# Kernel tuning notes

Hardware: AMD Instinct MI355X
Metric: run time of the kernel (lower is better)

## Reference

```python
import jax, jax.numpy as jnp
import numpy as np

N_NODES = 50000
N_EDGES = 800000
MAX_ITER = 20  # torchdeq default f_max_iter=40; fixed iteration count for a tractable jit-able baseline
K = 3          # TAGConv default number of hops
INS, EMB, HID, OUT = 4, 64, 128, 1


def setup_inputs():
    key = jax.random.key(0)
    ks = jax.random.split(key, 12)
    def lin(k, fan_in, fan_out):
        return jax.random.normal(k, (fan_in, fan_out), jnp.float32) / np.sqrt(fan_in)
    def tag_w(k, fan_in, fan_out):
        # stacked weights for the K+1 TAGConv linear maps: [K+1, in, out]
        return jax.random.normal(k, (K + 1, fan_in, fan_out), jnp.float32) / np.sqrt(fan_in * (K + 1))
    return {
        "x": jax.random.normal(ks[0], (N_NODES, INS), jnp.float32),
        "pos": jax.random.normal(ks[1], (N_NODES, 3), jnp.float32),
        "edge_attr": jax.random.uniform(ks[2], (N_EDGES,), jnp.float32),
        "up_w1": lin(ks[3], INS, EMB), "up_b1": jnp.zeros((EMB,), jnp.float32),
        "up_w2": lin(ks[4], EMB, EMB), "up_b2": jnp.zeros((EMB,), jnp.float32),
        "c1_w": tag_w(ks[5], EMB + 3, HID), "c1_b": jnp.zeros((HID,), jnp.float32),
        "c2_w": tag_w(ks[6], HID, HID), "c2_b": jnp.zeros((HID,), jnp.float32),
        "c3_w": tag_w(ks[7], HID, EMB), "c3_b": jnp.zeros((EMB,), jnp.float32),
        "down_w1": lin(ks[8], EMB, OUT), "down_b1": jnp.zeros((OUT,), jnp.float32),
        "down_w2": lin(ks[9], OUT, OUT), "down_b2": jnp.zeros((OUT,), jnp.float32),
        "edge_index": jax.random.randint(ks[10], (2, N_EDGES), 0, N_NODES, jnp.int32),
    }


def _gcn_norm(row, col, edge_attr, n):
    # PyG gcn_norm with edge weights, no self loops (TAGConv default)
    deg = jax.ops.segment_sum(edge_attr, col, num_segments=n)
    safe = jnp.where(deg > 0, deg, 1.0)
    dinv = jnp.where(deg > 0, jax.lax.rsqrt(safe), 0.0)
    return dinv[row] * edge_attr * dinv[col]


def _mlp(x, w1, b1, w2, b2):
    # torch F.gelu default = exact erf gelu
    return jax.nn.gelu(x @ w1 + b1, approximate=False) @ w2 + b2


def reference(x, pos, edge_attr, up_w1, up_b1, up_w2, up_b2, c1_w, c1_b, c2_w, c2_b, c3_w, c3_b, down_w1, down_b1, down_w2, down_b2, edge_index):
    n = x.shape[0]
    row, col = edge_index[0], edge_index[1]
    norm = _gcn_norm(row, col, edge_attr, n)

    def tag(h, W, b):
        # TAGConv: sum_k lin_k( A_hat^k x ) + bias
        out = h @ W[0]
        for k in range(1, W.shape[0]):
            h = jax.ops.segment_sum(h[row] * norm[:, None], col, num_segments=n)  # [E,C] gather-scatter
            out = out + h @ W[k]
        return out + b

    def gnn(z):
        h = jnp.concatenate([z, pos], axis=1)
        h = jax.nn.relu(tag(h, c1_w, c1_b))
        h = jax.nn.relu(tag(h, c2_w, c2_b))  # F.dropout is identity in eval mode
        h = tag(h, c3_w, c3_b)
        return jax.nn.log_softmax(h, axis=1)

    z0 = _mlp(x, up_w1, up_b1, up_w2, up_b2)
    z = jax.lax.fori_loop(0, MAX_ITER, lambda i, zz: gnn(zz), z0)  # fixed-point solver
    z_star = gnn(z)  # phantom-gradient step (torchdeq grad=1)
    out = _mlp(z_star, down_w1, down_b1, down_w2, down_b2)
    return out, z_star
```

## Files before the change

### kernel.cpp

```cpp
#include <hip/hip_runtime.h>
#include <hip/hip_bf16.h>

#define N_NODES 50000
#define N_EDGES 800000
#define MAX_ITER 20

typedef __attribute__((ext_vector_type(8))) short bf16x8;
typedef __attribute__((ext_vector_type(4))) float f32x4;

__device__ __forceinline__ float gelu_f(float x){
  return 0.5f*x*(1.0f+erff(x*0.70710678118654752f));
}
__device__ __forceinline__ ushort f2b(float f){
  uint x = __float_as_uint(f);
  uint r = (x + 0x7fffu + ((x>>16)&1u)) >> 16;
  return (ushort)r;
}

__global__ void deg_cnt_kernel(const int* __restrict__ col, const float* __restrict__ attr,
                               float* __restrict__ deg, int* __restrict__ cnt){
  int e = blockIdx.x*256 + threadIdx.x;
  if (e < N_EDGES){
    int c = col[e];
    atomicAdd(&deg[c], attr[e]);
    atomicAdd(&cnt[c], 1);
  }
}

__global__ void norm_kernel(const int* __restrict__ row, const int* __restrict__ col,
                            const float* __restrict__ attr, const float* __restrict__ deg,
                            float* __restrict__ nrm){
  int e = blockIdx.x*256 + threadIdx.x;
  if (e < N_EDGES){
    float dr = deg[row[e]], dc = deg[col[e]];
    float ir = dr > 0.f ? rsqrtf(dr) : 0.f;
    float ic = dc > 0.f ? rsqrtf(dc) : 0.f;
    nrm[e] = ir * attr[e] * ic;
  }
}

__global__ void scan_kernel(const int* __restrict__ cnt, int* __restrict__ starts,
                            int* __restrict__ cursor){
  __shared__ int buf[1024];
  __shared__ int carry;
  int tid = threadIdx.x;
  if (tid==0) carry = 0;
  __syncthreads();
  for (int base=0; base<N_NODES; base+=1024){
    int i = base+tid;
    int v = (i<N_NODES)? cnt[i] : 0;
    int cv = carry;
    buf[tid]=v;
    __syncthreads();
    for (int off=1; off<1024; off<<=1){
      int t = (tid>=off)? buf[tid-off] : 0;
      __syncthreads();
      buf[tid]+=t;
      __syncthreads();
    }
    int excl = buf[tid]-v+cv;
    if (i<N_NODES){ starts[i]=excl; cursor[i]=excl; }
    __syncthreads();
    if (tid==0) carry = cv + buf[1023];
    __syncthreads();
  }
  if (tid==0) starts[N_NODES] = carry;
}

__global__ void fill_kernel(const int* __restrict__ row, const int* __restrict__ col,
                            const float* __restrict__ nrm, int* __restrict__ cursor,
                            int* __restrict__ csr_row, float* __restrict__ csr_nrm){
  int e = blockIdx.x*256+threadIdx.x;
  if (e<N_EDGES){
    int c = col[e];
    int p = atomicAdd(&cursor[c],1);
    csr_row[p]=row[e];
    csr_nrm[p]=nrm[e];
  }
}

__global__ void pack_w1(const float* __restrict__ W, ushort* __restrict__ PB){
  int i = blockIdx.x*256+threadIdx.x;
  if (i < 4*8*128*8){
    int e = i&7; int n = (i>>3)&127; int kb = (i>>10)&7; int j = i>>13;
    int k = kb*8+e;
    PB[i] = f2b(W[((size_t)j*67 + k)*128 + n]);
  }
}
__global__ void pack_w2(const float* __restrict__ W, ushort* __restrict__ PB){
  int i = blockIdx.x*256+threadIdx.x;
  if (i < 4*16*128*8){
    int e = i&7; int n = (i>>3)&127; int kb = (i>>10)&15; int j = i>>14;
    int k = kb*8+e;
    PB[i] = f2b(W[((size_t)j*128 + k)*128 + n]);
  }
}
__global__ void pack_w3(const float* __restrict__ W, ushort* __restrict__ PB){
  int i = blockIdx.x*256+threadIdx.x;
  if (i < 16*256*8){
    int e = i&7; int n = (i>>3)&255; int kb = i>>11;
    int k = kb*8+e;
    PB[i] = f2b(W[(((size_t)(n>>6))*128 + k)*64 + (n&63)]);
  }
}

__global__ __launch_bounds__(256) void mlp_up_kernel(
    const float* __restrict__ x, const float* __restrict__ w1, const float* __restrict__ b1,
    const float* __restrict__ w2, const float* __restrict__ b2, ushort* __restrict__ z){
  __shared__ float sw1[4*64];
  __shared__ float sw2[64*64];
  __shared__ float sb1[64], sb2[64];
  __shared__ float t1s[4][64];
  int tid = threadIdx.x;
  for (int i=tid;i<256;i+=256) sw1[i]=w1[i];
  for (int i=tid;i<4096;i+=256) sw2[i]=w2[i];
  if (tid<64){ sb1[tid]=b1[tid]; sb2[tid]=b2[tid]; }
  __syncthreads();
  int g = tid>>6;
  int c = tid&63;
  int node = blockIdx.x*4 + g;
  float acc = sb1[c];
  #pragma unroll
  for (int k=0;k<4;k++) acc += x[node*4+k]*sw1[k*64+c];
  t1s[g][c] = gelu_f(acc);
  __syncthreads();
  float acc2 = sb2[c];
  #pragma unroll 8
  for (int k=0;k<64;k++) acc2 += t1s[g][k]*sw2[k*64+c];
  z[(size_t)node*64+c] = f2b(acc2);
}

template<int LDIN>
__global__ void posprop(const float* __restrict__ in, float* __restrict__ out,
                        const int* __restrict__ starts, const int* __restrict__ crow,
                        const float* __restrict__ cnrm){
  int v = blockIdx.x*256+threadIdx.x;
  if (v >= N_NODES) return;
  int s=starts[v], e=starts[v+1];
  float a0=0.f,a1=0.f,a2=0.f;
  for (int i=s;i<e;++i){
    int r=crow[i]; float nm=cnrm[i];
    a0 = fmaf(in[(size_t)r*LDIN+0], nm, a0);
    a1 = fmaf(in[(size_t)r*LDIN+1], nm, a1);
    a2 = fmaf(in[(size_t)r*LDIN+2], nm, a2);
  }
  float4 o = {a0,a1,a2,0.f};
  *(float4*)(out + (size_t)v*4) = o;
}

__global__ __launch_bounds__(256) void posbias_kernel(
    const float* __restrict__ pos, const float* __restrict__ P1,
    const float* __restrict__ P2, const float* __restrict__ P3,
    const float* __restrict__ c1w, const float* __restrict__ c1b,
    ushort* __restrict__ pb){
  __shared__ float sw[4][3][128];
  int tid=threadIdx.x;
  for (int i=tid; i<4*3*128; i+=256){
    int cc=i&127; int d=(i>>7)%3; int j=i/(3*128);
    sw[j][d][cc] = c1w[((size_t)j*67 + 64 + d)*128 + cc];
  }
  __syncthreads();
  int idx = blockIdx.x*256+tid;
  if (idx < N_NODES*128){
    int n = idx>>7, cc = idx&127;
    float a = c1b[cc];
    #pragma unroll
    for (int d=0;d<3;d++) a = fmaf(pos[(size_t)n*3+d], sw[0][d][cc], a);
    #pragma unroll
    for (int d=0;d<3;d++) a = fmaf(P1[(size_t)n*4+d], sw[1][d][cc], a);
    #pragma unroll
    for (int d=0;d<3;d++) a = fmaf(P2[(size_t)n*4+d], sw[2][d][cc], a);
    #pragma unroll
    for (int d=0;d<3;d++) a = fmaf(P3[(size_t)n*4+d], sw[3][d][cc], a);
    pb[idx]=f2b(a);
  }
}

__global__ __launch_bounds__(256) void prop128(
    const ushort* __restrict__ h, ushort* __restrict__ out,
    const int* __restrict__ starts, const int* __restrict__ crow,
    const float* __restrict__ cnrm){
  int wv = threadIdx.x >> 6;
  int v = blockIdx.x*4 + wv;
  int t = threadIdx.x & 63;
  int g = t >> 4;
  int c = t & 15;
  int s = starts[v], e = starts[v+1];
  float acc[8] = {0,0,0,0,0,0,0,0};
  for (int i=s; i<e; i+=64){
    int cnt = e - i; if (cnt > 64) cnt = 64;
    int r = 0; float nm = 0.f;
    if (t < cnt){ r = crow[i+t]; nm = cnrm[i+t]; }
    for (int jb=0; jb<cnt; jb+=4){
      int rr  = __shfl(r,  jb+g, 64);
      float w = __shfl(nm, jb+g, 64);
      uint4 hv = *(const uint4*)(h + (size_t)rr*128 + c*8);
      const uint* hp = (const uint*)&hv;
      #pragma unroll
      for (int q=0;q<4;q++){
        acc[2*q]   = fmaf(__uint_as_float(hp[q]<<16),          w, acc[2*q]);
        acc[2*q+1] = fmaf(__uint_as_float(hp[q]&0xffff0000u),  w, acc[2*q+1]);
      }
    }
  }
  #pragma unroll
  for (int q=0;q<8;q++){
    acc[q] += __shfl_xor(acc[q], 16, 64);
    acc[q] += __shfl_xor(acc[q], 32, 64);
  }
  if (g==0){
    uint4 o; uint* op=(uint*)&o;
    #pragma unroll
    for (int q=0;q<4;q++) op[q] = (uint)f2b(acc[2*q]) | ((uint)f2b(acc[2*q+1])<<16);
    *(uint4*)(out + (size_t)v*128 + c*8) = o;
  }
}

template<int MODE>
__global__ __launch_bounds__(256) void prop64(
    const ushort* __restrict__ h, void* __restrict__ outp,
    const ushort* __restrict__ adj, const float* __restrict__ bias,
    const int* __restrict__ starts, const int* __restrict__ crow,
    const float* __restrict__ cnrm){
  int wv = threadIdx.x >> 6;
  int v = blockIdx.x*4 + wv;
  int t = threadIdx.x & 63;
  int g = t >> 3;
  int c = t & 7;
  int s = starts[v], e = starts[v+1];
  float acc[8] = {0,0,0,0,0,0,0,0};
  for (int i=s; i<e; i+=64){
    int cnt = e - i; if (cnt > 64) cnt = 64;
    int r = 0; float nm = 0.f;
    if (t < cnt){ r = crow[i+t]; nm = cnrm[i+t]; }
    for (int jb=0; jb<cnt; jb+=8){
      int rr  = __shfl(r,  jb+g, 64);
      float w = __shfl(nm, jb+g, 64);
      uint4 hv = *(const uint4*)(h + (size_t)rr*64 + c*8);
      const uint* hp = (const uint*)&hv;
      #pragma unroll
      for (int q=0;q<4;q++){
        acc[2*q]   = fmaf(__uint_as_float(hp[q]<<16),          w, acc[2*q]);
        acc[2*q+1] = fmaf(__uint_as_float(hp[q]&0xffff0000u),  w, acc[2*q+1]);
      }
    }
  }
  #pragma unroll
  for (int q=0;q<8;q++){
    acc[q] += __shfl_xor(acc[q], 8, 64);
    acc[q] += __shfl_xor(acc[q], 16, 64);
    acc[q] += __shfl_xor(acc[q], 32, 64);
  }
  if (MODE==0){
    if (g==0){
      uint4 o; uint* op=(uint*)&o;
      #pragma unroll
      for (int q=0;q<4;q++) op[q] = (uint)f2b(acc[2*q]) | ((uint)f2b(acc[2*q+1])<<16);
      *(uint4*)((ushort*)outp + (size_t)v*64 + c*8) = o;
    }
  } else if (MODE==1){
    if (g==0){
      uint4 av = *(const uint4*)(adj + (size_t)v*64 + c*8);
      const uint* ap=(const uint*)&av;
      uint4 o; uint* op=(uint*)&o;
      #pragma unroll
      for (int q=0;q<4;q++){
        float lo = acc[2*q]   + __uint_as_float(ap[q]<<16);
        float hi = acc[2*q+1] + __uint_as_float(ap[q]&0xffff0000u);
        op[q] = (uint)f2b(lo) | ((uint)f2b(hi)<<16);
      }
      *(uint4*)((ushort*)outp + (size_t)v*64 + c*8) = o;
    }
  } else {
    uint4 av = *(const uint4*)(adj + (size_t)v*64 + c*8);
    const uint* ap=(const uint*)&av;
    float vv[8];
    #pragma unroll
    for (int q=0;q<4;q++){
      vv[2*q]   = acc[2*q]   + __uint_as_float(ap[q]<<16)         + bias[c*8+2*q];
      vv[2*q+1] = acc[2*q+1] + __uint_as_float(ap[q]&0xffff0000u) + bias[c*8+2*q+1];
    }
    float m = vv[0];
    #pragma unroll
    for (int q=1;q<8;q++) m = fmaxf(m, vv[q]);
    m = fmaxf(m, __shfl_xor(m,1,64));
    m = fmaxf(m, __shfl_xor(m,2,64));
    m = fmaxf(m, __shfl_xor(m,4,64));
    float ssum = 0.f;
    #pragma unroll
    for (int q=0;q<8;q++) ssum += __expf(vv[q]-m);
    ssum += __shfl_xor(ssum,1,64);
    ssum += __shfl_xor(ssum,2,64);
    ssum += __shfl_xor(ssum,4,64);
    float lse = m + __logf(ssum);
    if (g==0){
      if (MODE==2){
        uint4 o; uint* op=(uint*)&o;
        #pragma unroll
        for (int q=0;q<4;q++) op[q] = (uint)f2b(vv[2*q]-lse) | ((uint)f2b(vv[2*q+1]-lse)<<16);
        *(uint4*)((ushort*)outp + (size_t)v*64 + c*8) = o;
      } else {
        float* zo = (float*)outp + (size_t)v*64 + c*8;
        #pragma unroll
        for (int q=0;q<8;q++) zo[q] = vv[q]-lse;
      }
    }
  }
}

template<int KC, bool PERNODE_BIAS>
__global__ __launch_bounds__(256) void gemm4in(
    const ushort* __restrict__ H0, const ushort* __restrict__ H1,
    const ushort* __restrict__ H2, const ushort* __restrict__ H3,
    const ushort* __restrict__ PB, const void* __restrict__ biasp,
    ushort* __restrict__ out){
  constexpr int NT = 8;
  constexpr int NKS = KC/32;
  int lane = threadIdx.x & 63;
  int wv   = threadIdx.x >> 6;
  int m0 = blockIdx.x*64 + wv*16;
  int lr = lane & 15, lg = lane >> 4;
  int arow = m0 + lr; if (arow > N_NODES-1) arow = N_NODES-1;
  const ushort* Hs[4] = {H0,H1,H2,H3};
  f32x4 acc[NT];
  #pragma unroll
  for (int t=0;t<NT;t++) acc[t] = (f32x4){0.f,0.f,0.f,0.f};
  #pragma unroll
  for (int j=0;j<4;j++){
    const ushort* Hj  = Hs[j] + (size_t)arow*KC + lg*8;
    const ushort* PBj = PB + (size_t)j*(KC/8)*128*8;
    #pragma unroll
    for (int ks=0; ks<NKS; ks++){
      bf16x8 af = *(const bf16x8*)(Hj + ks*32);
      int kb = ks*4 + lg;
      #pragma unroll
      for (int t=0;t<NT;t++){
        bf16x8 bf = *(const bf16x8*)(PBj + ((size_t)kb*128 + t*16 + lr)*8);
        acc[t] = __builtin_amdgcn_mfma_f32_16x16x32_bf16(af, bf, acc[t], 0, 0, 0);
      }
    }
  }
  #pragma unroll
  for (int t=0;t<NT;t++){
    #pragma unroll
    for (int q=0;q<4;q++){
      int node = m0 + lg*4 + q;
      if (node < N_NODES){
        int col = t*16 + lr;
        float b;
        if (PERNODE_BIAS) b = __uint_as_float(((uint)((const ushort*)biasp)[(size_t)node*128+col])<<16);
        else              b = ((const float*)biasp)[col];
        float vo = fmaxf(acc[t][q] + b, 0.f);
        out[(size_t)node*128 + col] = f2b(vo);
      }
    }
  }
}

__global__ __launch_bounds__(256) void gemm_y(
    const ushort* __restrict__ T2, const ushort* __restrict__ PB,
    ushort* __restrict__ Y){
  constexpr int NT = 16;
  int lane = threadIdx.x & 63;
  int wv   = threadIdx.x >> 6;
  int m0 = blockIdx.x*64 + wv*16;
  int lr = lane & 15, lg = lane >> 4;
  int arow = m0 + lr; if (arow > N_NODES-1) arow = N_NODES-1;
  f32x4 acc[NT];
  #pragma unroll
  for (int t=0;t<NT;t++) acc[t] = (f32x4){0.f,0.f,0.f,0.f};
  const ushort* Hj = T2 + (size_t)arow*128 + lg*8;
  #pragma unroll
  for (int ks=0; ks<4; ks++){
    bf16x8 af = *(const bf16x8*)(Hj + ks*32);
    int kb = ks*4 + lg;
    #pragma unroll
    for (int t=0;t<NT;t++){
      bf16x8 bf = *(const bf16x8*)(PB + ((size_t)kb*256 + t*16 + lr)*8);
      acc[t] = __builtin_amdgcn_mfma_f32_16x16x32_bf16(af, bf, acc[t], 0, 0, 0);
    }
  }
  #pragma unroll
  for (int t=0;t<NT;t++){
    int n = t*16 + lr;
    int j = n >> 6, cc = n & 63;
    #pragma unroll
    for (int q=0;q<4;q++){
      int node = m0 + lg*4 + q;
      if (node < N_NODES)
        Y[(size_t)j*N_NODES*64 + (size_t)node*64 + cc] = f2b(acc[t][q]);
    }
  }
}

__global__ __launch_bounds__(256) void mlp_down_kernel(
    const float* __restrict__ zs, const float* __restrict__ dw1, const float* __restrict__ db1,
    const float* __restrict__ dw2, const float* __restrict__ db2, float* __restrict__ out){
  int node = blockIdx.x*4 + (threadIdx.x>>6);
  int c = threadIdx.x & 63;
  float v = zs[(size_t)node*64+c]*dw1[c];
  #pragma unroll
  for (int off=32; off; off>>=1) v += __shfl_xor(v, off, 64);
  if (c==0) out[node] = gelu_f(v + db1[0]) * dw2[0] + db2[0];
}

extern "C" void kernel_launch(void* const* d_in, const int* in_sizes, int n_in,
                              void* d_out, int out_size, void* d_ws, size_t ws_size,
                              hipStream_t stream){
  const float* x     = (const float*)d_in[0];
  const float* pos   = (const float*)d_in[1];
  const float* eattr = (const float*)d_in[2];
  const float* up_w1 = (const float*)d_in[3];
  const float* up_b1 = (const float*)d_in[4];
  const float* up_w2 = (const float*)d_in[5];
  const float* up_b2 = (const float*)d_in[6];
  const float* c1_w  = (const float*)d_in[7];
  const float* c1_b  = (const float*)d_in[8];
  const float* c2_w  = (const float*)d_in[9];
  const float* c2_b  = (const float*)d_in[10];
  const float* c3_w  = (const float*)d_in[11];
  const float* c3_b  = (const float*)d_in[12];
  const float* dw1   = (const float*)d_in[13];
  const float* db1   = (const float*)d_in[14];
  const float* dw2   = (const float*)d_in[15];
  const float* db2   = (const float*)d_in[16];
  const int*   eidx  = (const int*)d_in[17];
  const int* row = eidx;
  const int* col = eidx + N_EDGES;

  char* wsp = (char*)d_ws;
  size_t off = 0;
  auto alloc = [&](size_t bytes)->char*{
    char* p = wsp + off;
    off = (off + bytes + 255) & ~(size_t)255;
    return p;
  };
  float*  deg    = (float*)alloc((size_t)N_NODES*4);
  int*    cnt    = (int*)  alloc((size_t)N_NODES*4);
  int*    starts = (int*)  alloc((size_t)(N_NODES+1)*4);
  int*    cursor = (int*)  alloc((size_t)N_NODES*4);
  float*  nrm    = (float*)alloc((size_t)N_EDGES*4);
  int*    crow   = (int*)  alloc((size_t)N_EDGES*4);
  float*  cnrm   = (float*)alloc((size_t)N_EDGES*4);
  float*  P1     = (float*)alloc((size_t)N_NODES*4*4);
  float*  P2     = (float*)alloc((size_t)N_NODES*4*4);
  float*  P3     = (float*)alloc((size_t)N_NODES*4*4);
  ushort* pbias  = (ushort*)alloc((size_t)N_NODES*128*2);
  ushort* z      = (ushort*)alloc((size_t)N_NODES*64*2);
  ushort* q1     = (ushort*)alloc((size_t)N_NODES*64*2);
  ushort* q2     = (ushort*)alloc((size_t)N_NODES*64*2);
  ushort* q3     = (ushort*)alloc((size_t)N_NODES*64*2);
  ushort* t1     = (ushort*)alloc((size_t)N_NODES*128*2);
  ushort* p1     = (ushort*)alloc((size_t)N_NODES*128*2);
  ushort* p2     = (ushort*)alloc((size_t)N_NODES*128*2);
  ushort* p3     = (ushort*)alloc((size_t)N_NODES*128*2);
  ushort* t2     = (ushort*)alloc((size_t)N_NODES*128*2);
  ushort* PB1    = (ushort*)alloc((size_t)4*8*128*8*2);
  ushort* PB2    = (ushort*)alloc((size_t)4*16*128*8*2);
  ushort* PB3    = (ushort*)alloc((size_t)16*256*8*2);

  ushort* Y  = p1;
  ushort* Y0 = Y;
  ushort* Y1 = Y + (size_t)1*N_NODES*64;
  ushort* Y2 = Y + (size_t)2*N_NODES*64;
  ushort* Y3 = Y + (size_t)3*N_NODES*64;
  ushort* u1 = q1;
  ushort* u2 = q2;

  float* outv  = (float*)d_out;
  float* zstar = (float*)d_out + N_NODES;

  hipMemsetAsync(deg, 0, (size_t)N_NODES*4, stream);
  hipMemsetAsync(cnt, 0, (size_t)N_NODES*4, stream);
  int eb = (N_EDGES+255)/256;
  deg_cnt_kernel<<<eb,256,0,stream>>>(col, eattr, deg, cnt);
  norm_kernel<<<eb,256,0,stream>>>(row, col, eattr, deg, nrm);
  scan_kernel<<<1,1024,0,stream>>>(cnt, starts, cursor);
  fill_kernel<<<eb,256,0,stream>>>(row, col, nrm, cursor, crow, cnrm);
  pack_w1<<<128,256,0,stream>>>(c1_w, PB1);
  pack_w2<<<256,256,0,stream>>>(c2_w, PB2);
  pack_w3<<<128,256,0,stream>>>(c3_w, PB3);
  mlp_up_kernel<<<N_NODES/4,256,0,stream>>>(x, up_w1, up_b1, up_w2, up_b2, z);

  int nb = (N_NODES+255)/256;
  posprop<3><<<nb,256,0,stream>>>(pos, P1, starts, crow, cnrm);
  posprop<4><<<nb,256,0,stream>>>(P1,  P2, starts, crow, cnrm);
  posprop<4><<<nb,256,0,stream>>>(P2,  P3, starts, crow, cnrm);
  posbias_kernel<<<(N_NODES*128)/256,256,0,stream>>>(pos, P1, P2, P3, c1_w, c1_b, pbias);

  const int gprop = N_NODES/4;
  const int ggemm = (N_NODES+63)/64;

  for (int it=0; it<=MAX_ITER; ++it){
    prop64<0><<<gprop,256,0,stream>>>(z,  q1, nullptr, nullptr, starts, crow, cnrm);
    prop64<0><<<gprop,256,0,stream>>>(q1, q2, nullptr, nullptr, starts, crow, cnrm);
    prop64<0><<<gprop,256,0,stream>>>(q2, q3, nullptr, nullptr, starts, crow, cnrm);
    gemm4in<64,true><<<ggemm,256,0,stream>>>(z,q1,q2,q3,PB1,pbias,t1);

    prop128<<<gprop,256,0,stream>>>(t1,p1,starts,crow,cnrm);
    prop128<<<gprop,256,0,stream>>>(p1,p2,starts,crow,cnrm);
    prop128<<<gprop,256,0,stream>>>(p2,p3,starts,crow,cnrm);
    gemm4in<128,false><<<ggemm,256,0,stream>>>(t1,p1,p2,p3,PB2,c2_b,t2);

    gemm_y<<<ggemm,256,0,stream>>>(t2, PB3, Y);
    prop64<1><<<gprop,256,0,stream>>>(Y3, u1, Y2, nullptr, starts, crow, cnrm);
    prop64<1><<<gprop,256,0,stream>>>(u1, u2, Y1, nullptr, starts, crow, cnrm);
    if (it < MAX_ITER){
      prop64<2><<<gprop,256,0,stream>>>(u2, z, Y0, c3_b, starts, crow, cnrm);
    } else {
      prop64<3><<<gprop,256,0,stream>>>(u2, zstar, Y0, c3_b, starts, crow, cnrm);
    }
  }
  mlp_down_kernel<<<N_NODES/4,256,0,stream>>>(zstar, dw1, db1, dw2, db2, outv);
}
```

Measured before the change: 7.227 ms.

## Pack CSR edges into int2, use grid-stride propagation with 2-edge ILP, 32-row GEMM tiles

CSR row index and norm are interleaved into one int2 array, so each edge needs a single 8-byte load. The propagation kernels switch to a fixed 2048-block grid-stride loop and replace shuffle broadcasts with direct per-lane edge loads, two edges at a time, to get more gathers in flight. The GEMM kernels now give each wave two 16-row tiles so every B-fragment load feeds two MFMAs. The costs are more registers per thread and possible load imbalance from the fixed grid.

```diff
diff --git a/kernel.cpp b/kernel.cpp
--- a/kernel.cpp
+++ b/kernel.cpp
@@ -4,6 +4,7 @@
 #define N_NODES 50000
 #define N_EDGES 800000
 #define MAX_ITER 20
+#define PROP_GRID 2048
 
 typedef __attribute__((ext_vector_type(8))) short bf16x8;
 typedef __attribute__((ext_vector_type(4))) float f32x4;
@@ -69,13 +70,12 @@
 
 __global__ void fill_kernel(const int* __restrict__ row, const int* __restrict__ col,
                             const float* __restrict__ nrm, int* __restrict__ cursor,
-                            int* __restrict__ csr_row, float* __restrict__ csr_nrm){
+                            int2* __restrict__ ep){
   int e = blockIdx.x*256+threadIdx.x;
   if (e<N_EDGES){
     int c = col[e];
     int p = atomicAdd(&cursor[c],1);
-    csr_row[p]=row[e];
-    csr_nrm[p]=nrm[e];
+    ep[p] = make_int2(row[e], __float_as_int(nrm[e]));
   }
 }
 
@@ -132,17 +132,17 @@
 
 template<int LDIN>
 __global__ void posprop(const float* __restrict__ in, float* __restrict__ out,
-                        const int* __restrict__ starts, const int* __restrict__ crow,
-                        const float* __restrict__ cnrm){
+                        const int* __restrict__ starts, const int2* __restrict__ ep){
   int v = blockIdx.x*256+threadIdx.x;
   if (v >= N_NODES) return;
   int s=starts[v], e=starts[v+1];
   float a0=0.f,a1=0.f,a2=0.f;
   for (int i=s;i<e;++i){
-    int r=crow[i]; float nm=cnrm[i];
-    a0 = fmaf(in[(size_t)r*LDIN+0], nm, a0);
-    a1 = fmaf(in[(size_t)r*LDIN+1], nm, a1);
-    a2 = fmaf(in[(size_t)r*LDIN+2], nm, a2);
+    int2 ed = ep[i];
+    float nm = __int_as_float(ed.y);
+    a0 = fmaf(in[(size_t)ed.x*LDIN+0], nm, a0);
+    a1 = fmaf(in[(size_t)ed.x*LDIN+1], nm, a1);
+    a2 = fmaf(in[(size_t)ed.x*LDIN+2], nm, a2);
   }
   float4 o = {a0,a1,a2,0.f};
   *(float4*)(out + (size_t)v*4) = o;
@@ -178,41 +178,43 @@
 
 __global__ __launch_bounds__(256) void prop128(
     const ushort* __restrict__ h, ushort* __restrict__ out,
-    const int* __restrict__ starts, const int* __restrict__ crow,
-    const float* __restrict__ cnrm){
+    const int* __restrict__ starts, const int2* __restrict__ ep){
   int wv = threadIdx.x >> 6;
-  int v = blockIdx.x*4 + wv;
   int t = threadIdx.x & 63;
   int g = t >> 4;
   int c = t & 15;
-  int s = starts[v], e = starts[v+1];
-  float acc[8] = {0,0,0,0,0,0,0,0};
-  for (int i=s; i<e; i+=64){
-    int cnt = e - i; if (cnt > 64) cnt = 64;
-    int r = 0; float nm = 0.f;
-    if (t < cnt){ r = crow[i+t]; nm = cnrm[i+t]; }
-    for (int jb=0; jb<cnt; jb+=4){
-      int rr  = __shfl(r,  jb+g, 64);
-      float w = __shfl(nm, jb+g, 64);
-      uint4 hv = *(const uint4*)(h + (size_t)rr*128 + c*8);
-      const uint* hp = (const uint*)&hv;
+  for (int v = blockIdx.x*4 + wv; v < N_NODES; v += PROP_GRID*4){
+    int s = starts[v], e = starts[v+1];
+    float acc[8] = {0,0,0,0,0,0,0,0};
+    for (int i=s; i<e; i+=8){
+      int iA = i + g, iB = i + 4 + g;
+      int2 eA = make_int2(0,0), eB = make_int2(0,0);
+      if (iA < e) eA = ep[iA];
+      if (iB < e) eB = ep[iB];
+      float wA = __int_as_float(eA.y), wB = __int_as_float(eB.y);
+      uint4 hA = *(const uint4*)(h + (size_t)eA.x*128 + c*8);
+      uint4 hB = *(const uint4*)(h + (size_t)eB.x*128 + c*8);
+      const uint* pA = (const uint*)&hA;
+      const uint* pB = (const uint*)&hB;
       #pragma unroll
       for (int q=0;q<4;q++){
-        acc[2*q]   = fmaf(__uint_as_float(hp[q]<<16),          w, acc[2*q]);
-        acc[2*q+1] = fmaf(__uint_as_float(hp[q]&0xffff0000u),  w, acc[2*q+1]);
-      }
-    }
-  }
-  #pragma unroll
-  for (int q=0;q<8;q++){
-    acc[q] += __shfl_xor(acc[q], 16, 64);
-    acc[q] += __shfl_xor(acc[q], 32, 64);
-  }
-  if (g==0){
-    uint4 o; uint* op=(uint*)&o;
-    #pragma unroll
-    for (int q=0;q<4;q++) op[q] = (uint)f2b(acc[2*q]) | ((uint)f2b(acc[2*q+1])<<16);
-    *(uint4*)(out + (size_t)v*128 + c*8) = o;
+        acc[2*q]   = fmaf(__uint_as_float(pA[q]<<16),         wA, acc[2*q]);
+        acc[2*q+1] = fmaf(__uint_as_float(pA[q]&0xffff0000u), wA, acc[2*q+1]);
+        acc[2*q]   = fmaf(__uint_as_float(pB[q]<<16),         wB, acc[2*q]);
+        acc[2*q+1] = fmaf(__uint_as_float(pB[q]&0xffff0000u), wB, acc[2*q+1]);
+      }
+    }
+    #pragma unroll
+    for (int q=0;q<8;q++){
+      acc[q] += __shfl_xor(acc[q], 16, 64);
+      acc[q] += __shfl_xor(acc[q], 32, 64);
+    }
+    if (g==0){
+      uint4 o; uint* op=(uint*)&o;
+      #pragma unroll
+      for (int q=0;q<4;q++) op[q] = (uint)f2b(acc[2*q]) | ((uint)f2b(acc[2*q+1])<<16);
+      *(uint4*)(out + (size_t)v*128 + c*8) = o;
+    }
   }
 }
 
@@ -220,89 +222,93 @@
 __global__ __launch_bounds__(256) void prop64(
     const ushort* __restrict__ h, void* __restrict__ outp,
     const ushort* __restrict__ adj, const float* __restrict__ bias,
-    const int* __restrict__ starts, const int* __restrict__ crow,
-    const float* __restrict__ cnrm){
+    const int* __restrict__ starts, const int2* __restrict__ ep){
   int wv = threadIdx.x >> 6;
-  int v = blockIdx.x*4 + wv;
   int t = threadIdx.x & 63;
   int g = t >> 3;
   int c = t & 7;
-  int s = starts[v], e = starts[v+1];
-  float acc[8] = {0,0,0,0,0,0,0,0};
-  for (int i=s; i<e; i+=64){
-    int cnt = e - i; if (cnt > 64) cnt = 64;
-    int r = 0; float nm = 0.f;
-    if (t < cnt){ r = crow[i+t]; nm = cnrm[i+t]; }
-    for (int jb=0; jb<cnt; jb+=8){
-      int rr  = __shfl(r,  jb+g, 64);
-      float w = __shfl(nm, jb+g, 64);
-      uint4 hv = *(const uint4*)(h + (size_t)rr*64 + c*8);
-      const uint* hp = (const uint*)&hv;
+  for (int v = blockIdx.x*4 + wv; v < N_NODES; v += PROP_GRID*4){
+    int s = starts[v], e = starts[v+1];
+    float acc[8] = {0,0,0,0,0,0,0,0};
+    for (int i=s; i<e; i+=16){
+      int iA = i + g, iB = i + 8 + g;
+      int2 eA = make_int2(0,0), eB = make_int2(0,0);
+      if (iA < e) eA = ep[iA];
+      if (iB < e) eB = ep[iB];
+      float wA = __int_as_float(eA.y), wB = __int_as_float(eB.y);
+      uint4 hA = *(const uint4*)(h + (size_t)eA.x*64 + c*8);
+      uint4 hB = *(const uint4*)(h + (size_t)eB.x*64 + c*8);
+      const uint* pA = (const uint*)&hA;
+      const uint* pB = (const uint*)&hB;
       #pragma unroll
       for (int q=0;q<4;q++){
-        acc[2*q]   = fmaf(__uint_as_float(hp[q]<<16),          w, acc[2*q]);
-        acc[2*q+1] = fmaf(__uint_as_float(hp[q]&0xffff0000u),  w, acc[2*q+1]);
-      }
-    }
-  }
-  #pragma unroll
-  for (int q=0;q<8;q++){
-    acc[q] += __shfl_xor(acc[q], 8, 64);
-    acc[q] += __shfl_xor(acc[q], 16, 64);
-    acc[q] += __shfl_xor(acc[q], 32, 64);
-  }
-  if (MODE==0){
-    if (g==0){
-      uint4 o; uint* op=(uint*)&o;
-      #pragma unroll
-      for (int q=0;q<4;q++) op[q] = (uint)f2b(acc[2*q]) | ((uint)f2b(acc[2*q+1])<<16);
-      *(uint4*)((ushort*)outp + (size_t)v*64 + c*8) = o;
-    }
-  } else if (MODE==1){
-    if (g==0){
+        acc[2*q]   = fmaf(__uint_as_float(pA[q]<<16),         wA, acc[2*q]);
+        acc[2*q+1] = fmaf(__uint_as_float(pA[q]&0xffff0000u), wA, acc[2*q+1]);
+        acc[2*q]   = fmaf(__uint_as_float(pB[q]<<16),         wB, acc[2*q]);
+        acc[2*q+1] = fmaf(__uint_as_float(pB[q]&0xffff0000u), wB, acc[2*q+1]);
+      }
+    }
+    #pragma unroll
+    for (int q=0;q<8;q++){
+      acc[q] += __shfl_xor(acc[q], 8, 64);
+      acc[q] += __shfl_xor(acc[q], 16, 64);
+      acc[q] += __shfl_xor(acc[q], 32, 64);
+    }
+    if (MODE==0){
+      if (g==0){
+        uint4 o; uint* op=(uint*)&o;
+        #pragma unroll
+        for (int q=0;q<4;q++) op[q] = (uint)f2b(acc[2*q]) | ((uint)f2b(acc[2*q+1])<<16);
+        *(uint4*)((ushort*)outp + (size_t)v*64 + c*8) = o;
+      }
+    } else if (MODE==1){
+      if (g==0){
+        uint4 av = *(const uint4*)(adj + (size_t)v*64 + c*8);
+        const uint* ap=(const uint*)&av;
+        uint4 o; uint* op=(uint*)&o;
+        #pragma unroll
+        for (int q=0;q<4;q++){
+          float lo = acc[2*q]   + __uint_as_float(ap[q]<<16);
+          float hi = acc[2*q+1] + __uint_as_float(ap[q]&0xffff0000u);
+          op[q] = (uint)f2b(lo) | ((uint)f2b(hi)<<16);
+        }
+        *(uint4*)((ushort*)outp + (size_t)v*64 + c*8) = o;
+      }
+    } else {
       uint4 av = *(const uint4*)(adj + (size_t)v*64 + c*8);
       const uint* ap=(const uint*)&av;
-      uint4 o; uint* op=(uint*)&o;
+      float vv[8];
       #pragma unroll
       for (int q=0;q<4;q++){
-        float lo = acc[2*q]   + __uint_as_float(ap[q]<<16);
-        float hi = acc[2*q+1] + __uint_as_float(ap[q]&0xffff0000u);
-        op[q] = (uint)f2b(lo) | ((uint)f2b(hi)<<16);
-      }
-      *(uint4*)((ushort*)outp + (size_t)v*64 + c*8) = o;
-    }
-  } else {
-    uint4 av = *(const uint4*)(adj + (size_t)v*64 + c*8);
-    const uint* ap=(const uint*)&av;
-    float vv[8];
-    #pragma unroll
-    for (int q=0;q<4;q++){
-      vv[2*q]   = acc[2*q]   + __uint_as_float(ap[q]<<16)         + bias[c*8+2*q];
-      vv[2*q+1] = acc[2*q+1] + __uint_as_float(ap[q]&0xffff0000u) + bias[c*8+2*q+1];
-    }
-    float m = vv[0];
-    #pragma unroll
-    for (int q=1;q<8;q++) m = fmaxf(m, vv[q]);
-    m = fmaxf(m, __shfl_xor(m,1,64));
-    m = fmaxf(m, __shfl_xor(m,2,64));
-    m = fmaxf(m, __shfl_xor(m,4,64));
-    float ssum = 0.f;
-    #pragma unroll
-    for (int q=0;q<8;q++) ssum += __expf(vv[q]-m);
-    ssum += __shfl_xor(ssum,1,64);
-    ssum += __shfl_xor(ssum,2,64);
-    ssum += __shfl_xor(ssum,4,64);
-    float lse = m + __logf(ssum);
-    if (g==0){
-      if (MODE==2){
-        uint4 o; uint* op=(uint*)&o;
-        #pragma unroll
-        for (int q=0;q<4;q++) op[q] = (uint)f2b(vv[2*q]-lse) | ((uint)f2b(vv[2*q+1]-lse)<<16);
-        *(uint4*)((ushort*)outp + (size_t)v*64 + c*8) = o;
-      } else {
-        float* zo = (float*)outp + (size_t)v*64 + c*8;
-        #pragma unroll
-        for (int q=0;q<8;q++) zo[q] = vv[q]-lse;
+        vv[2*q]   = acc[2*q]   + __uint_as_float(ap[q]<<16)         + bias[c*8+2*q];
+        vv[2*q+1] = acc[2*q+1] + __uint_as_float(ap[q]&0xffff0000u) + bias[c*8+2*q+1];
+      }
+      float m = vv[0];
+      #pragma unroll
+      for (int q=1;q<8;q++) m = fmaxf(m, vv[q]);
+      m = fmaxf(m, __shfl_xor(m,1,64));
+      m = fmaxf(m, __shfl_xor(m,2,64));
+      m = fmaxf(m, __shfl_xor(m,4,64));
+      float ssum = 0.f;
+      #pragma unroll
+      for (int q=0;q<8;q++) ssum += __expf(vv[q]-m);
+      ssum += __shfl_xor(ssum,1,64);
+      ssum += __shfl_xor(ssum,2,64);
+      ssum += __shfl_xor(ssum,4,64);
+      float lse = m + __logf(ssum);
+      if (g==0){
+        if (MODE==2){
+          uint4 o; uint* op=(uint*)&o;
+          #pragma unroll
+          for (int q=0;q<4;q++) op[q] = (uint)f2b(vv[2*q]-lse) | ((uint)f2b(vv[2*q+1]-lse)<<16);
+          *(uint4*)((ushort*)outp + (size_t)v*64 + c*8) = o;
+        } else {
+          float* zo = (float*)outp + (size_t)v*64 + c*8;
+          float4 o0 = {vv[0]-lse, vv[1]-lse, vv[2]-lse, vv[3]-lse};
+          float4 o1 = {vv[4]-lse, vv[5]-lse, vv[6]-lse, vv[7]-lse};
+          *(float4*)zo = o0;
+          *(float4*)(zo+4) = o1;
+        }
       }
     }
   }
@@ -318,40 +324,49 @@
   constexpr int NKS = KC/32;
   int lane = threadIdx.x & 63;
   int wv   = threadIdx.x >> 6;
-  int m0 = blockIdx.x*64 + wv*16;
+  int m0 = blockIdx.x*128 + wv*32;
   int lr = lane & 15, lg = lane >> 4;
-  int arow = m0 + lr; if (arow > N_NODES-1) arow = N_NODES-1;
+  int ar0 = min(m0 + lr,      N_NODES-1);
+  int ar1 = min(m0 + 16 + lr, N_NODES-1);
   const ushort* Hs[4] = {H0,H1,H2,H3};
-  f32x4 acc[NT];
-  #pragma unroll
-  for (int t=0;t<NT;t++) acc[t] = (f32x4){0.f,0.f,0.f,0.f};
+  f32x4 acc[2][NT];
+  #pragma unroll
+  for (int rt=0;rt<2;rt++)
+    #pragma unroll
+    for (int t=0;t<NT;t++) acc[rt][t] = (f32x4){0.f,0.f,0.f,0.f};
   #pragma unroll
   for (int j=0;j<4;j++){
-    const ushort* Hj  = Hs[j] + (size_t)arow*KC + lg*8;
+    const ushort* Hj0 = Hs[j] + (size_t)ar0*KC + lg*8;
+    const ushort* Hj1 = Hs[j] + (size_t)ar1*KC + lg*8;
     const ushort* PBj = PB + (size_t)j*(KC/8)*128*8;
     #pragma unroll
     for (int ks=0; ks<NKS; ks++){
-      bf16x8 af = *(const bf16x8*)(Hj + ks*32);
+      bf16x8 a0 = *(const bf16x8*)(Hj0 + ks*32);
+      bf16x8 a1 = *(const bf16x8*)(Hj1 + ks*32);
       int kb = ks*4 + lg;
       #pragma unroll
       for (int t=0;t<NT;t++){
         bf16x8 bf = *(const bf16x8*)(PBj + ((size_t)kb*128 + t*16 + lr)*8);
-        acc[t] = __builtin_amdgcn_mfma_f32_16x16x32_bf16(af, bf, acc[t], 0, 0, 0);
-      }
-    }
-  }
-  #pragma unroll
-  for (int t=0;t<NT;t++){
-    #pragma unroll
-    for (int q=0;q<4;q++){
-      int node = m0 + lg*4 + q;
-      if (node < N_NODES){
-        int col = t*16 + lr;
-        float b;
-        if (PERNODE_BIAS) b = __uint_as_float(((uint)((const ushort*)biasp)[(size_t)node*128+col])<<16);
-        else              b = ((const float*)biasp)[col];
-        float vo = fmaxf(acc[t][q] + b, 0.f);
-        out[(size_t)node*128 + col] = f2b(vo);
+        acc[0][t] = __builtin_amdgcn_mfma_f32_16x16x32_bf16(a0, bf, acc[0][t], 0, 0, 0);
+        acc[1][t] = __builtin_amdgcn_mfma_f32_16x16x32_bf16(a1, bf, acc[1][t], 0, 0, 0);
+      }
+    }
+  }
+  #pragma unroll
+  for (int rt=0;rt<2;rt++){
+    #pragma unroll
+    for (int t=0;t<NT;t++){
+      #pragma unroll
+      for (int q=0;q<4;q++){
+        int node = m0 + rt*16 + lg*4 + q;
+        if (node < N_NODES){
+          int col = t*16 + lr;
+          float b;
+          if (PERNODE_BIAS) b = __uint_as_float(((uint)((const ushort*)biasp)[(size_t)node*128+col])<<16);
+          else              b = ((const float*)biasp)[col];
+          float vo = fmaxf(acc[rt][t][q] + b, 0.f);
+          out[(size_t)node*128 + col] = f2b(vo);
+        }
       }
     }
   }
@@ -363,32 +378,41 @@
   constexpr int NT = 16;
   int lane = threadIdx.x & 63;
   int wv   = threadIdx.x >> 6;
-  int m0 = blockIdx.x*64 + wv*16;
+  int m0 = blockIdx.x*128 + wv*32;
   int lr = lane & 15, lg = lane >> 4;
-  int arow = m0 + lr; if (arow > N_NODES-1) arow = N_NODES-1;
-  f32x4 acc[NT];
-  #pragma unroll
-  for (int t=0;t<NT;t++) acc[t] = (f32x4){0.f,0.f,0.f,0.f};
-  const ushort* Hj = T2 + (size_t)arow*128 + lg*8;
+  int ar0 = min(m0 + lr,      N_NODES-1);
+  int ar1 = min(m0 + 16 + lr, N_NODES-1);
+  f32x4 acc[2][NT];
+  #pragma unroll
+  for (int rt=0;rt<2;rt++)
+    #pragma unroll
+    for (int t=0;t<NT;t++) acc[rt][t] = (f32x4){0.f,0.f,0.f,0.f};
+  const ushort* H0 = T2 + (size_t)ar0*128 + lg*8;
+  const ushort* H1 = T2 + (size_t)ar1*128 + lg*8;
   #pragma unroll
   for (int ks=0; ks<4; ks++){
-    bf16x8 af = *(const bf16x8*)(Hj + ks*32);
+    bf16x8 a0 = *(const bf16x8*)(H0 + ks*32);
+    bf16x8 a1 = *(const bf16x8*)(H1 + ks*32);
     int kb = ks*4 + lg;
     #pragma unroll
     for (int t=0;t<NT;t++){
       bf16x8 bf = *(const bf16x8*)(PB + ((size_t)kb*256 + t*16 + lr)*8);
-      acc[t] = __builtin_amdgcn_mfma_f32_16x16x32_bf16(af, bf, acc[t], 0, 0, 0);
-    }
-  }
-  #pragma unroll
-  for (int t=0;t<NT;t++){
-    int n = t*16 + lr;
-    int j = n >> 6, cc = n & 63;
-    #pragma unroll
-    for (int q=0;q<4;q++){
-      int node = m0 + lg*4 + q;
-      if (node < N_NODES)
-        Y[(size_t)j*N_NODES*64 + (size_t)node*64 + cc] = f2b(acc[t][q]);
+      acc[0][t] = __builtin_amdgcn_mfma_f32_16x16x32_bf16(a0, bf, acc[0][t], 0, 0, 0);
+      acc[1][t] = __builtin_amdgcn_mfma_f32_16x16x32_bf16(a1, bf, acc[1][t], 0, 0, 0);
+    }
+  }
+  #pragma unroll
+  for (int rt=0;rt<2;rt++){
+    #pragma unroll
+    for (int t=0;t<NT;t++){
+      int n = t*16 + lr;
+      int j = n >> 6, cc = n & 63;
+      #pragma unroll
+      for (int q=0;q<4;q++){
+        int node = m0 + rt*16 + lg*4 + q;
+        if (node < N_NODES)
+          Y[(size_t)j*N_NODES*64 + (size_t)node*64 + cc] = f2b(acc[rt][t][q]);
+      }
     }
   }
 }
@@ -440,8 +464,7 @@
   int*    starts = (int*)  alloc((size_t)(N_NODES+1)*4);
   int*    cursor = (int*)  alloc((size_t)N_NODES*4);
   float*  nrm    = (float*)alloc((size_t)N_EDGES*4);
-  int*    crow   = (int*)  alloc((size_t)N_EDGES*4);
-  float*  cnrm   = (float*)alloc((size_t)N_EDGES*4);
+  int2*   ep     = (int2*) alloc((size_t)N_EDGES*8);
   float*  P1     = (float*)alloc((size_t)N_NODES*4*4);
   float*  P2     = (float*)alloc((size_t)N_NODES*4*4);
   float*  P3     = (float*)alloc((size_t)N_NODES*4*4);
@@ -476,39 +499,38 @@
   deg_cnt_kernel<<<eb,256,0,stream>>>(col, eattr, deg, cnt);
   norm_kernel<<<eb,256,0,stream>>>(row, col, eattr, deg, nrm);
   scan_kernel<<<1,1024,0,stream>>>(cnt, starts, cursor);
-  fill_kernel<<<eb,256,0,stream>>>(row, col, nrm, cursor, crow, cnrm);
+  fill_kernel<<<eb,256,0,stream>>>(row, col, nrm, cursor, ep);
   pack_w1<<<128,256,0,stream>>>(c1_w, PB1);
   pack_w2<<<256,256,0,stream>>>(c2_w, PB2);
   pack_w3<<<128,256,0,stream>>>(c3_w, PB3);
   mlp_up_kernel<<<N_NODES/4,256,0,stream>>>(x, up_w1, up_b1, up_w2, up_b2, z);
 
   int nb = (N_NODES+255)/256;
-  posprop<3><<<nb,256,0,stream>>>(pos, P1, starts, crow, cnrm);
-  posprop<4><<<nb,256,0,stream>>>(P1,  P2, starts, crow, cnrm);
-  posprop<4><<<nb,256,0,stream>>>(P2,  P3, starts, crow, cnrm);
+  posprop<3><<<nb,256,0,stream>>>(pos, P1, starts, ep);
+  posprop<4><<<nb,256,0,stream>>>(P1,  P2, starts, ep);
+  posprop<4><<<nb,256,0,stream>>>(P2,  P3, starts, ep);
   posbias_kernel<<<(N_NODES*128)/256,256,0,stream>>>(pos, P1, P2, P3, c1_w, c1_b, pbias);
 
-  const int gprop = N_NODES/4;
-  const int ggemm = (N_NODES+63)/64;
+  const int ggemm = (N_NODES+127)/128;
 
   for (int it=0; it<=MAX_ITER; ++it){
-    prop64<0><<<gprop,256,0,stream>>>(z,  q1, nullptr, nullptr, starts, crow, cnrm);
-    prop64<0><<<gprop,256,0,stream>>>(q1, q2, nullptr, nullptr, starts, crow, cnrm);
-    prop64<0><<<gprop,256,0,stream>>>(q2, q3, nullptr, nullptr, starts, crow, cnrm);
+    prop64<0><<<PROP_GRID,256,0,stream>>>(z,  q1, nullptr, nullptr, starts, ep);
+    prop64<0><<<PROP_GRID,256,0,stream>>>(q1, q2, nullptr, nullptr, starts, ep);
+    prop64<0><<<PROP_GRID,256,0,stream>>>(q2, q3, nullptr, nullptr, starts, ep);
     gemm4in<64,true><<<ggemm,256,0,stream>>>(z,q1,q2,q3,PB1,pbias,t1);
 
-    prop128<<<gprop,256,0,stream>>>(t1,p1,starts,crow,cnrm);
-    prop128<<<gprop,256,0,stream>>>(p1,p2,starts,crow,cnrm);
-    prop128<<<gprop,256,0,stream>>>(p2,p3,starts,crow,cnrm);
+    prop128<<<PROP_GRID,256,0,stream>>>(t1,p1,starts,ep);
+    prop128<<<PROP_GRID,256,0,stream>>>(p1,p2,starts,ep);
+    prop128<<<PROP_GRID,256,0,stream>>>(p2,p3,starts,ep);
     gemm4in<128,false><<<ggemm,256,0,stream>>>(t1,p1,p2,p3,PB2,c2_b,t2);
 
     gemm_y<<<ggemm,256,0,stream>>>(t2, PB3, Y);
-    prop64<1><<<gprop,256,0,stream>>>(Y3, u1, Y2, nullptr, starts, crow, cnrm);
-    prop64<1><<<gprop,256,0,stream>>>(u1, u2, Y1, nullptr, starts, crow, cnrm);
+    prop64<1><<<PROP_GRID,256,0,stream>>>(Y3, u1, Y2, nullptr, starts, ep);
+    prop64<1><<<PROP_GRID,256,0,stream>>>(u1, u2, Y1, nullptr, starts, ep);
     if (it < MAX_ITER){
-      prop64<2><<<gprop,256,0,stream>>>(u2, z, Y0, c3_b, starts, crow, cnrm);
+      prop64<2><<<PROP_GRID,256,0,stream>>>(u2, z, Y0, c3_b, starts, ep);
     } else {
-      prop64<3><<<gprop,256,0,stream>>>(u2, zstar, Y0, c3_b, starts, crow, cnrm);
+      prop64<3><<<PROP_GRID,256,0,stream>>>(u2, zstar, Y0, c3_b, starts, ep);
     }
   }
   mlp_down_kernel<<<N_NODES/4,256,0,stream>>>(zstar, dw1, db1, dw2, db2, outv);
```

Result: slower. 7.532 ms (+4.2%).
